# Kernel optimization log

Hardware: AMD Instinct MI355X
Metric: run time of the kernel (lower is better)

The kernel has to match this reference:

```python
import jax, jax.numpy as jnp
import numpy as np

B, T, D = 8, 2048, 1024
NUM_HEADS = 16
SCALE = 1.0 / np.sqrt(D // NUM_HEADS).astype(np.float32)  # sqrt(d_modal//num_heads), per source


def setup_inputs() -> dict:
    key = jax.random.key(0)
    ks = jax.random.split(key, 7)
    s = 1.0 / np.sqrt(D).astype(np.float32)
    return {
        "x": jax.random.normal(ks[0], (B, T, D), dtype=jnp.float32),
        "Wq_w": jax.random.normal(ks[1], (D, D), dtype=jnp.float32) * s,
        "Wq_b": jax.random.normal(ks[2], (D,), dtype=jnp.float32) * 0.01,
        "Wk_w": jax.random.normal(ks[3], (D, D), dtype=jnp.float32) * s,
        "Wk_b": jax.random.normal(ks[4], (D,), dtype=jnp.float32) * 0.01,
        "Wv_w": jax.random.normal(ks[5], (D, D), dtype=jnp.float32) * s,
        "Wv_b": jax.random.normal(ks[6], (D,), dtype=jnp.float32) * 0.01,
    }


def reference(x, Wq_w, Wq_b, Wk_w, Wk_b, Wv_w, Wv_b):
    # Linear projections (torch nn.Linear: y = x @ W.T + b)
    Q = jnp.einsum('btd,ed->bte', x, Wq_w) + Wq_b
    K = jnp.einsum('btd,ed->bte', x, Wk_w) + Wk_b
    V = jnp.einsum('btd,ed->bte', x, Wv_w) + Wv_b
    # scores [B, T, T], scaled by 1/sqrt(d_modal // num_heads) as in source
    scores = jnp.einsum('bqd,bkd->bqk', Q, K) * SCALE
    causal = jnp.tril(jnp.ones((T, T), dtype=bool))  # tril mask buffer
    scores = jnp.where(causal, scores, -jnp.inf)
    attn = jax.nn.softmax(scores, axis=-1)
    return jnp.einsum('bqk,bkd->bqd', attn, V)
```

## Files before the change

kernel.cpp:

```cpp
#include <hip/hip_runtime.h>


typedef float f32x4 __attribute__((ext_vector_type(4)));
typedef _Float16 half8 __attribute__((ext_vector_type(8)));

#define DEVINL __device__ __forceinline__
static constexpr float ATT_SCALE = 0.125f;

DEVINL void gload_lds16(const _Float16* g, _Float16* l) {
  __builtin_amdgcn_global_load_lds((const __attribute__((address_space(1))) void*)g,
                                   (__attribute__((address_space(3))) void*)l, 16, 0, 0);
}

#define SBAR() __builtin_amdgcn_sched_barrier(0)
#define MM(AOFF, BOFF, ASET, BSET) \
  _Pragma("unroll") for (int kk_ = 0; kk_ < 2; ++kk_) \
  _Pragma("unroll") for (int i_ = 0; i_ < 4; ++i_) \
  _Pragma("unroll") for (int jj_ = 0; jj_ < 2; ++jj_) \
    acc[(AOFF) + i_][(BOFF) + jj_] = __builtin_amdgcn_mfma_f32_16x16x32_f16( \
        ASET[i_][kk_], BSET[jj_][kk_], acc[(AOFF) + i_][(BOFF) + jj_], 0, 0, 0);
#define PH_BAR() SBAR(); __builtin_amdgcn_s_barrier(); \
    __builtin_amdgcn_s_setprio(1)
#define PH_DONE() __builtin_amdgcn_s_setprio(0); SBAR()

template <int LDA, int LDB, class GA, class GB>
DEVINL void gemm_core(GA ga, GB gb, int NT, char* ldsb, int tid, f32x4 acc[8][4]) {
  const int l = tid & 63, w = tid >> 6;
  const int wm = w >> 2, wn = w & 3;
  const int lr = l & 15, lk = l >> 4;
  int srow[2], scol[2];
#pragma unroll
  for (int i = 0; i < 2; ++i) {
    const int P = i * 512 + w * 64 + l;
    srow[i] = P >> 3;
    scol[i] = (P & 7) ^ (srow[i] & 7);
  }
  const int ch0 = ((lk ^ (lr & 7)) << 4);
  const int ch1 = (((lk + 4) ^ (lr & 7)) << 4);
  const int abase = lr * 128;
  const int bbase = (wn & 1) * 8192 + lr * 128;

  half8 aA[4][2], aB[4][2], bA[2][2], bB[2][2];

  auto STGA = [&](int t, int h, int bufb) {
    const _Float16* g0 = ga(t, h);
    char* dst = ldsb + bufb * 65536 + h * 16384;
#pragma unroll
    for (int i = 0; i < 2; ++i)
      gload_lds16(g0 + (size_t)srow[i] * LDA + scol[i] * 8,
                  (_Float16*)(dst + i * 8192 + w * 1024));
  };
  auto STGB = [&](int t, int h, int bufb) {
    const _Float16* g0 = gb(t, h);
    char* dst = ldsb + bufb * 65536 + 32768 + h * 16384;
#pragma unroll
    for (int i = 0; i < 2; ++i)
      gload_lds16(g0 + (size_t)srow[i] * LDB + scol[i] * 8,
                  (_Float16*)(dst + i * 8192 + w * 1024));
  };
  auto RDA = [&](int bufb, int ih, half8 d[4][2]) {
    const char* sA = ldsb + bufb * 65536 + wm * 16384 + ih * 8192;
#pragma unroll
    for (int i = 0; i < 4; ++i) {
      d[i][0] = *(const half8*)(sA + abase + i * 2048 + ch0);
      d[i][1] = *(const half8*)(sA + abase + i * 2048 + ch1);
    }
  };
  auto RDB = [&](int bufb, int jh, half8 d[2][2]) {
    const char* sB = ldsb + bufb * 65536 + 32768 + (wn >> 1) * 16384 + jh * 4096;
#pragma unroll
    for (int jj = 0; jj < 2; ++jj) {
      d[jj][0] = *(const half8*)(sB + bbase + jj * 2048 + ch0);
      d[jj][1] = *(const half8*)(sB + bbase + jj * 2048 + ch1);
    }
  };

  auto tile = [&](int t, bool stA, bool stB) {
    const int bufb = t & 1, obuf = bufb ^ 1;
    RDB(bufb, 1, bB);
    if (stA) STGA(t + 1, 0, obuf);
    PH_BAR(); MM(0, 0, aA, bA); PH_DONE();
    RDA(bufb, 1, aB);
    if (stA) STGA(t + 1, 1, obuf);
    PH_BAR(); MM(0, 2, aA, bB); PH_DONE();
    if (stB) STGB(t + 2, 0, bufb);
    SBAR();
    if (stB)      { asm volatile("s_waitcnt vmcnt(2)" ::: "memory"); }
    else if (stA) { asm volatile("s_waitcnt vmcnt(0)" ::: "memory"); }
    PH_BAR(); MM(4, 0, aB, bA); PH_DONE();
    if (stA) { RDA(obuf, 0, aA); RDB(obuf, 0, bA); }
    if (stB) STGB(t + 2, 1, bufb);
    PH_BAR(); MM(4, 2, aB, bB); PH_DONE();
  };

  STGA(0, 0, 0); STGA(0, 1, 0); STGB(0, 0, 0); STGB(0, 1, 0);
  STGB(1, 0, 1); STGB(1, 1, 1);
  asm volatile("s_waitcnt vmcnt(4)" ::: "memory");
  __builtin_amdgcn_s_barrier(); SBAR();
  RDA(0, 0, aA); RDB(0, 0, bA);
  for (int t = 0; t < NT - 2; ++t) tile(t, true, true);
  tile(NT - 2, true, false);
  tile(NT - 1, false, false);
}

__global__ __launch_bounds__(256) void cvt_all(const float* __restrict__ x,
                                               const float* __restrict__ wq,
                                               const float* __restrict__ wk,
                                               const float* __restrict__ wv,
                                               _Float16* __restrict__ xh,
                                               _Float16* __restrict__ wqh,
                                               _Float16* __restrict__ wkh,
                                               _Float16* __restrict__ wvh) {
  const int n8 = 2490368;
  for (int i = blockIdx.x * 256 + threadIdx.x; i < n8; i += 2048 * 256) {
    const float* src; _Float16* dst; int off;
    if (i < 2097152)      { src = x;  dst = xh;  off = i; }
    else if (i < 2228224) { src = wq; dst = wqh; off = i - 2097152; }
    else if (i < 2359296) { src = wk; dst = wkh; off = i - 2228224; }
    else                  { src = wv; dst = wvh; off = i - 2359296; }
    const float4* p = (const float4*)src + (size_t)off * 2;
    float4 v0 = p[0], v1 = p[1];
    half8 h;
    h[0] = (_Float16)v0.x; h[1] = (_Float16)v0.y; h[2] = (_Float16)v0.z; h[3] = (_Float16)v0.w;
    h[4] = (_Float16)v1.x; h[5] = (_Float16)v1.y; h[6] = (_Float16)v1.z; h[7] = (_Float16)v1.w;
    *((half8*)dst + off) = h;
  }
}

__global__ __launch_bounds__(512) void gemm_qkv(
    const _Float16* __restrict__ xh, const _Float16* __restrict__ Wqh,
    const _Float16* __restrict__ Wkh, const _Float16* __restrict__ Wvh,
    const float* __restrict__ bq, const float* __restrict__ bk,
    const float* __restrict__ bv, _Float16* __restrict__ Qh,
    _Float16* __restrict__ Kh, _Float16* __restrict__ VT) {
  __shared__ _Float16 lds[65536];
  const int tid = threadIdx.x;
  const int bid = blockIdx.x;
  const int swz = (bid & 7) * 96 + (bid >> 3);
  const int mt = swz / 12, nt = swz % 12;
  const int sel = nt >> 2;
  const _Float16* Wsel = sel == 0 ? Wqh : (sel == 1 ? Wkh : Wvh);
  const float* bsel = sel == 0 ? bq : (sel == 1 ? bk : bv);
  const _Float16* Ab = xh + (size_t)mt * 256 * 1024;
  const _Float16* Bb = Wsel + (size_t)(nt & 3) * 256 * 1024;
  f32x4 acc[8][4] = {};
  auto ga = [&](int t, int h) { return Ab + (size_t)h * 128 * 1024 + t * 64; };
  auto gb = [&](int t, int h) { return Bb + (size_t)h * 128 * 1024 + t * 64; };
  gemm_core<1024, 1024>(ga, gb, 16, (char*)lds, tid, acc);
  const int l = tid & 63, w = tid >> 6;
  const int wm = w >> 2, wn = w & 3;
  const int lr = l & 15, lk = l >> 4;
  const int n0 = (nt & 3) * 256;
  __syncthreads();
#pragma unroll
  for (int ai = 0; ai < 8; ++ai) {
    const int rbase = wm * 128 + (ai >> 2) * 64 + (ai & 3) * 16 + lk * 4;
#pragma unroll
    for (int j = 0; j < 4; ++j) {
      const int col = wn * 64 + j * 16 + lr;
      const float bvv = bsel[n0 + col];
#pragma unroll
      for (int r = 0; r < 4; ++r) {
        const int row = rbase + r;
        const float v = acc[ai][j][r] + bvv;
        if (sel < 2)
          lds[row * 256 + ((col + (row >> 2) * 16) & 255)] = (_Float16)v;
        else
          lds[col * 256 + ((row + (col >> 2) * 16) & 255)] = (_Float16)v;
      }
    }
  }
  __syncthreads();
#pragma unroll
  for (int i = 0; i < 16; ++i) {
    const int c = i * 512 + tid;
    const int row = c >> 5, c8 = c & 31;
    half8 v = *(const half8*)&lds[row * 256 + ((c8 * 8 + (row >> 2) * 16) & 255)];
    if (sel < 2) {
      _Float16* Out = sel == 0 ? Qh : Kh;
      *(half8*)&Out[(size_t)(mt * 256 + row) * 1024 + n0 + c8 * 8] = v;
    } else {
      const int bb = mt >> 3, t0 = (mt & 7) * 256;
      *(half8*)&VT[((size_t)bb * 1024 + n0 + row) * 2048 + t0 + c8 * 8] = v;
    }
  }
}

__global__ __launch_bounds__(512) void gemm_qk(const _Float16* __restrict__ Qh,
                                               const _Float16* __restrict__ Kh,
                                               float* __restrict__ Sc) {
  __shared__ _Float16 lds[65536];
  const int tid = threadIdx.x;
  const int idx = blockIdx.x, bb = blockIdx.y;
  int qt = 0;
  while ((qt + 1) * (qt + 2) / 2 <= idx) ++qt;
  const int jt = idx - qt * (qt + 1) / 2;
  const _Float16* Ab = Qh + ((size_t)bb * 2048 + qt * 256) * 1024;
  const _Float16* Bb = Kh + ((size_t)bb * 2048 + jt * 256) * 1024;
  f32x4 acc[8][4] = {};
  auto ga = [&](int t, int h) { return Ab + (size_t)h * 128 * 1024 + t * 64; };
  auto gb = [&](int t, int h) { return Bb + (size_t)h * 128 * 1024 + t * 64; };
  gemm_core<1024, 1024>(ga, gb, 16, (char*)lds, tid, acc);
  const int l = tid & 63, w = tid >> 6;
  const int wm = w >> 2, wn = w & 3;
  const int lr = l & 15, lk = l >> 4;
  float* St = Sc + ((size_t)bb * 36 + idx) * 65536;
  const float NINF = -__builtin_inff();
#pragma unroll
  for (int ai = 0; ai < 8; ++ai) {
    const int rbase = wm * 128 + (ai >> 2) * 64 + (ai & 3) * 16 + lk * 4;
#pragma unroll
    for (int j = 0; j < 4; ++j) {
      const int ck = wn * 64 + j * 16 + lr;
      const int kg = jt * 256 + ck;
#pragma unroll
      for (int r = 0; r < 4; ++r) {
        const int rq = rbase + r;
        const int qg = qt * 256 + rq;
        St[(size_t)rq * 256 + ck] = (kg <= qg) ? acc[ai][j][r] * ATT_SCALE : NINF;
      }
    }
  }
}

__global__ __launch_bounds__(256) void softmax_p(const float* __restrict__ Sc,
                                                 _Float16* __restrict__ Pc) {
  const int l = threadIdx.x & 63;
  const int gid = blockIdx.x * 4 + (threadIdx.x >> 6);
  const int b = gid >> 11, q = gid & 2047;
  const int qt = q >> 8, rq = q & 255;
  const int ntile = qt + 1;
  const size_t base = ((size_t)b * 36 + (size_t)(qt * (qt + 1) / 2)) * 65536 +
                      (size_t)rq * 256 + l * 4;
  float vx[32];
  float m = -__builtin_inff();
#pragma unroll
  for (int c = 0; c < 8; ++c) {
    float4 t = {-__builtin_inff(), -__builtin_inff(), -__builtin_inff(), -__builtin_inff()};
    if (c < ntile) t = *(const float4*)&Sc[base + (size_t)c * 65536];
    vx[4 * c] = t.x; vx[4 * c + 1] = t.y; vx[4 * c + 2] = t.z; vx[4 * c + 3] = t.w;
    m = fmaxf(m, fmaxf(fmaxf(t.x, t.y), fmaxf(t.z, t.w)));
  }
#pragma unroll
  for (int s = 1; s < 64; s <<= 1) m = fmaxf(m, __shfl_xor(m, s, 64));
  float sum = 0.f;
#pragma unroll
  for (int i = 0; i < 32; ++i) { vx[i] = __expf(vx[i] - m); sum += vx[i]; }
#pragma unroll
  for (int s = 1; s < 64; s <<= 1) sum += __shfl_xor(sum, s, 64);
  const float inv = 1.f / sum;
  _Float16* Pb = Pc + base;
#pragma unroll
  for (int c = 0; c < 8; ++c) {
    if (c < ntile) {
      _Float16 tmp[4];
      tmp[0] = (_Float16)(vx[4 * c] * inv);
      tmp[1] = (_Float16)(vx[4 * c + 1] * inv);
      tmp[2] = (_Float16)(vx[4 * c + 2] * inv);
      tmp[3] = (_Float16)(vx[4 * c + 3] * inv);
      *(uint64_t*)&Pb[(size_t)c * 65536] = *(const uint64_t*)tmp;
    }
  }
}

__global__ __launch_bounds__(512) void gemm_pv(const _Float16* __restrict__ Pc,
                                               const _Float16* __restrict__ VT,
                                               float* __restrict__ O) {
  __shared__ _Float16 lds[65536];
  const int tid = threadIdx.x;
  const int dt = blockIdx.x, qt = 7 - blockIdx.y, b = blockIdx.z;
  const _Float16* Pb = Pc + ((size_t)b * 36 + (size_t)(qt * (qt + 1) / 2)) * 65536;
  const _Float16* Vb = VT + ((size_t)b * 1024 + dt * 256) * 2048;
  f32x4 acc[8][4] = {};
  auto ga = [&](int t, int h) {
    return Pb + (size_t)(t >> 2) * 65536 + (size_t)h * 128 * 256 + (t & 3) * 64;
  };
  auto gb = [&](int t, int h) { return Vb + (size_t)h * 128 * 2048 + t * 64; };
  gemm_core<256, 2048>(ga, gb, (qt + 1) * 4, (char*)lds, tid, acc);
  const int l = tid & 63, w = tid >> 6;
  const int wm = w >> 2, wn = w & 3;
  const int lr = l & 15, lk = l >> 4;
#pragma unroll
  for (int ai = 0; ai < 8; ++ai) {
    const int rbase = qt * 256 + wm * 128 + (ai >> 2) * 64 + (ai & 3) * 16 + lk * 4;
#pragma unroll
    for (int j = 0; j < 4; ++j) {
      const int cg = dt * 256 + wn * 64 + j * 16 + lr;
#pragma unroll
      for (int r = 0; r < 4; ++r)
        O[((size_t)b * 2048 + rbase + r) * 1024 + cg] = acc[ai][j][r];
    }
  }
}

extern "C" void kernel_launch(void* const* d_in, const int* in_sizes, int n_in,
                              void* d_out, int out_size, void* d_ws, size_t ws_size,
                              hipStream_t stream) {
  const float* x    = (const float*)d_in[0];
  const float* Wq_w = (const float*)d_in[1];
  const float* Wq_b = (const float*)d_in[2];
  const float* Wk_w = (const float*)d_in[3];
  const float* Wk_b = (const float*)d_in[4];
  const float* Wv_w = (const float*)d_in[5];
  const float* Wv_b = (const float*)d_in[6];
  float* out = (float*)d_out;
  char* ws = (char*)d_ws;
  _Float16* xh  = (_Float16*)(ws);
  _Float16* Wqh = (_Float16*)(ws + 33554432);
  _Float16* Wkh = (_Float16*)(ws + 35651584);
  _Float16* Wvh = (_Float16*)(ws + 37748736);
  float*    Sc  = (float*)(ws);
  _Float16* Qh  = (_Float16*)(ws + 75497472);
  _Float16* Kh  = (_Float16*)(ws + 109051904);
  _Float16* Pc  = (_Float16*)(ws + 75497472);
  _Float16* VT  = (_Float16*)(ws + 142606336);

  cvt_all<<<2048, 256, 0, stream>>>(x, Wq_w, Wk_w, Wv_w, xh, Wqh, Wkh, Wvh);
  gemm_qkv<<<768, 512, 0, stream>>>(xh, Wqh, Wkh, Wvh, Wq_b, Wk_b, Wv_b, Qh, Kh, VT);
  gemm_qk<<<dim3(36, 8), 512, 0, stream>>>(Qh, Kh, Sc);
  softmax_p<<<4096, 256, 0, stream>>>(Sc, Pc);
  gemm_pv<<<dim3(4, 8, 8), 512, 0, stream>>>(Pc, VT, out);
}
```

Baseline: 283.8 us.

## Use 256x128 GEMM tiles for QK and PV, store scores as fp16

Adds a new GEMM core with 256x128 output tiles and a simpler double-buffered loop. The QK and PV kernels now use it, which doubles their grid sizes (576 and 512 blocks) for better CU occupancy and load balance on the causal triangle. The score matrix is written and read as fp16 instead of fp32, halving the intermediate traffic through softmax. The trade-offs are lower arithmetic intensity per tile, more barriers per k-step, and reduced precision of the pre-softmax scores.

```diff
diff --git a/kernel.cpp b/kernel.cpp
--- a/kernel.cpp
+++ b/kernel.cpp
@@ -3,6 +3,7 @@
 
 typedef float f32x4 __attribute__((ext_vector_type(4)));
 typedef _Float16 half8 __attribute__((ext_vector_type(8)));
+typedef _Float16 half4 __attribute__((ext_vector_type(4)));
 
 #define DEVINL __device__ __forceinline__
 static constexpr float ATT_SCALE = 0.125f;
@@ -13,6 +14,7 @@
 }
 
 #define SBAR() __builtin_amdgcn_sched_barrier(0)
+
 #define MM(AOFF, BOFF, ASET, BSET) \
   _Pragma("unroll") for (int kk_ = 0; kk_ < 2; ++kk_) \
   _Pragma("unroll") for (int i_ = 0; i_ < 4; ++i_) \
@@ -101,6 +103,88 @@
   for (int t = 0; t < NT - 2; ++t) tile(t, true, true);
   tile(NT - 2, true, false);
   tile(NT - 1, false, false);
+}
+
+template <int LDA, int LDB, class GA, class GB>
+DEVINL void gemm_n128(GA ga, GB gb, int NT, char* ldsb, int tid, f32x4 acc[4][4]) {
+  const int l = tid & 63, w = tid >> 6;
+  const int wm = w >> 1, wn = w & 1;
+  const int lr = l & 15, lk = l >> 4;
+  int srow[2], scol[2];
+#pragma unroll
+  for (int i = 0; i < 2; ++i) {
+    const int P = i * 512 + w * 64 + l;
+    srow[i] = P >> 3;
+    scol[i] = (P & 7) ^ (srow[i] & 7);
+  }
+  const int ch0 = ((lk ^ (lr & 7)) << 4);
+  const int ch1 = (((lk + 4) ^ (lr & 7)) << 4);
+  const int abase = (wm >> 1) * 16384 + ((wm & 1) * 64 + lr) * 128;
+  const int bbase = 32768 + (wn * 64 + lr) * 128;
+
+  auto STG = [&](const _Float16* g0, int ld, int bufb, int slot) {
+    char* dst = ldsb + bufb * 49152 + slot * 16384;
+#pragma unroll
+    for (int i = 0; i < 2; ++i)
+      gload_lds16(g0 + (size_t)srow[i] * ld + scol[i] * 8,
+                  (_Float16*)(dst + i * 8192 + w * 1024));
+  };
+  half8 a[4][2], bfr[4][2];
+  auto RD = [&](int bufb) {
+    const char* bb = ldsb + bufb * 49152;
+#pragma unroll
+    for (int i = 0; i < 4; ++i) {
+      a[i][0] = *(const half8*)(bb + abase + i * 2048 + ch0);
+      a[i][1] = *(const half8*)(bb + abase + i * 2048 + ch1);
+    }
+#pragma unroll
+    for (int j = 0; j < 4; ++j) {
+      bfr[j][0] = *(const half8*)(bb + bbase + j * 2048 + ch0);
+      bfr[j][1] = *(const half8*)(bb + bbase + j * 2048 + ch1);
+    }
+  };
+
+  STG(ga(0, 0), LDA, 0, 0); STG(ga(0, 1), LDA, 0, 1); STG(gb(0), LDB, 0, 2);
+  STG(ga(1, 0), LDA, 1, 0); STG(ga(1, 1), LDA, 1, 1); STG(gb(1), LDB, 1, 2);
+  asm volatile("s_waitcnt vmcnt(6)" ::: "memory");
+  __builtin_amdgcn_s_barrier();
+
+  for (int t = 0; t < NT; ++t) {
+    const int bufb = t & 1;
+    RD(bufb);
+    SBAR();
+    __builtin_amdgcn_s_barrier();
+    asm volatile("s_waitcnt lgkmcnt(0)" ::: "memory");
+    SBAR();
+    __builtin_amdgcn_s_setprio(1);
+#pragma unroll
+    for (int i = 0; i < 4; ++i)
+#pragma unroll
+      for (int j = 0; j < 4; ++j)
+        acc[i][j] = __builtin_amdgcn_mfma_f32_16x16x32_f16(a[i][0], bfr[j][0], acc[i][j], 0, 0, 0);
+    __builtin_amdgcn_s_setprio(0);
+    SBAR();
+    __builtin_amdgcn_s_barrier();
+    if (t + 2 < NT) {
+      STG(ga(t + 2, 0), LDA, bufb, 0);
+      STG(ga(t + 2, 1), LDA, bufb, 1);
+      STG(gb(t + 2), LDB, bufb, 2);
+      asm volatile("s_waitcnt vmcnt(6)" ::: "memory");
+    } else if (t + 1 < NT) {
+      asm volatile("s_waitcnt vmcnt(0)" ::: "memory");
+    }
+    SBAR();
+    __builtin_amdgcn_s_barrier();
+    __builtin_amdgcn_s_setprio(1);
+#pragma unroll
+    for (int i = 0; i < 4; ++i)
+#pragma unroll
+      for (int j = 0; j < 4; ++j)
+        acc[i][j] = __builtin_amdgcn_mfma_f32_16x16x32_f16(a[i][1], bfr[j][1], acc[i][j], 0, 0, 0);
+    __builtin_amdgcn_s_setprio(0);
+    SBAR();
+    __builtin_amdgcn_s_barrier();
+  }
 }
 
 __global__ __launch_bounds__(256) void cvt_all(const float* __restrict__ x,
@@ -188,42 +272,44 @@
 
 __global__ __launch_bounds__(512) void gemm_qk(const _Float16* __restrict__ Qh,
                                                const _Float16* __restrict__ Kh,
-                                               float* __restrict__ Sc) {
-  __shared__ _Float16 lds[65536];
+                                               _Float16* __restrict__ Sc) {
+  __shared__ _Float16 lds[49152];
   const int tid = threadIdx.x;
-  const int idx = blockIdx.x, bb = blockIdx.y;
-  int qt = 0;
-  while ((qt + 1) * (qt + 2) / 2 <= idx) ++qt;
-  const int jt = idx - qt * (qt + 1) / 2;
-  const _Float16* Ab = Qh + ((size_t)bb * 2048 + qt * 256) * 1024;
-  const _Float16* Bb = Kh + ((size_t)bb * 2048 + jt * 256) * 1024;
-  f32x4 acc[8][4] = {};
+  const int j = blockIdx.x;
+  const int b = j / 72, r = j % 72;
+  int qt = 0, cum = 0;
+  while (cum + (qt + 1) * 2 <= r) { cum += (qt + 1) * 2; ++qt; }
+  const int jn = r - cum;
+  const _Float16* Ab = Qh + ((size_t)b * 2048 + qt * 256) * 1024;
+  const _Float16* Bb = Kh + ((size_t)b * 2048 + jn * 128) * 1024;
+  f32x4 acc[4][4] = {};
   auto ga = [&](int t, int h) { return Ab + (size_t)h * 128 * 1024 + t * 64; };
-  auto gb = [&](int t, int h) { return Bb + (size_t)h * 128 * 1024 + t * 64; };
-  gemm_core<1024, 1024>(ga, gb, 16, (char*)lds, tid, acc);
+  auto gb = [&](int t) { return Bb + t * 64; };
+  gemm_n128<1024, 1024>(ga, gb, 16, (char*)lds, tid, acc);
   const int l = tid & 63, w = tid >> 6;
-  const int wm = w >> 2, wn = w & 3;
+  const int wm = w >> 1, wn = w & 1;
   const int lr = l & 15, lk = l >> 4;
-  float* St = Sc + ((size_t)bb * 36 + idx) * 65536;
-  const float NINF = -__builtin_inff();
-#pragma unroll
-  for (int ai = 0; ai < 8; ++ai) {
-    const int rbase = wm * 128 + (ai >> 2) * 64 + (ai & 3) * 16 + lk * 4;
-#pragma unroll
-    for (int j = 0; j < 4; ++j) {
-      const int ck = wn * 64 + j * 16 + lr;
-      const int kg = jt * 256 + ck;
-#pragma unroll
-      for (int r = 0; r < 4; ++r) {
-        const int rq = rbase + r;
-        const int qg = qt * 256 + rq;
-        St[(size_t)rq * 256 + ck] = (kg <= qg) ? acc[ai][j][r] * ATT_SCALE : NINF;
+  _Float16* St = Sc + ((size_t)b * 36 + (size_t)(qt * (qt + 1) / 2) + (jn >> 1)) * 65536 +
+                 (jn & 1) * 128;
+  const _Float16 NINF = (_Float16)(-__builtin_inff());
+#pragma unroll
+  for (int i = 0; i < 4; ++i) {
+#pragma unroll
+    for (int jj = 0; jj < 4; ++jj) {
+      const int col = wn * 64 + jj * 16 + lr;
+      const int kg = jn * 128 + col;
+#pragma unroll
+      for (int rr = 0; rr < 4; ++rr) {
+        const int row = wm * 64 + i * 16 + lk * 4 + rr;
+        const int qg = qt * 256 + row;
+        St[(size_t)row * 256 + col] =
+            (kg <= qg) ? (_Float16)(acc[i][jj][rr] * ATT_SCALE) : NINF;
       }
     }
   }
 }
 
-__global__ __launch_bounds__(256) void softmax_p(const float* __restrict__ Sc,
+__global__ __launch_bounds__(256) void softmax_p(const _Float16* __restrict__ Sc,
                                                  _Float16* __restrict__ Pc) {
   const int l = threadIdx.x & 63;
   const int gid = blockIdx.x * 4 + (threadIdx.x >> 6);
@@ -236,10 +322,13 @@
   float m = -__builtin_inff();
 #pragma unroll
   for (int c = 0; c < 8; ++c) {
-    float4 t = {-__builtin_inff(), -__builtin_inff(), -__builtin_inff(), -__builtin_inff()};
-    if (c < ntile) t = *(const float4*)&Sc[base + (size_t)c * 65536];
-    vx[4 * c] = t.x; vx[4 * c + 1] = t.y; vx[4 * c + 2] = t.z; vx[4 * c + 3] = t.w;
-    m = fmaxf(m, fmaxf(fmaxf(t.x, t.y), fmaxf(t.z, t.w)));
+    float x0 = -__builtin_inff(), x1 = x0, x2 = x0, x3 = x0;
+    if (c < ntile) {
+      half4 t = *(const half4*)&Sc[base + (size_t)c * 65536];
+      x0 = (float)t[0]; x1 = (float)t[1]; x2 = (float)t[2]; x3 = (float)t[3];
+    }
+    vx[4 * c] = x0; vx[4 * c + 1] = x1; vx[4 * c + 2] = x2; vx[4 * c + 3] = x3;
+    m = fmaxf(m, fmaxf(fmaxf(x0, x1), fmaxf(x2, x3)));
   }
 #pragma unroll
   for (int s = 1; s < 64; s <<= 1) m = fmaxf(m, __shfl_xor(m, s, 64));
@@ -253,12 +342,12 @@
 #pragma unroll
   for (int c = 0; c < 8; ++c) {
     if (c < ntile) {
-      _Float16 tmp[4];
-      tmp[0] = (_Float16)(vx[4 * c] * inv);
-      tmp[1] = (_Float16)(vx[4 * c + 1] * inv);
-      tmp[2] = (_Float16)(vx[4 * c + 2] * inv);
-      tmp[3] = (_Float16)(vx[4 * c + 3] * inv);
-      *(uint64_t*)&Pb[(size_t)c * 65536] = *(const uint64_t*)tmp;
+      half4 p;
+      p[0] = (_Float16)(vx[4 * c] * inv);
+      p[1] = (_Float16)(vx[4 * c + 1] * inv);
+      p[2] = (_Float16)(vx[4 * c + 2] * inv);
+      p[3] = (_Float16)(vx[4 * c + 3] * inv);
+      *(half4*)&Pb[(size_t)c * 65536] = p;
     }
   }
 }
@@ -266,29 +355,32 @@
 __global__ __launch_bounds__(512) void gemm_pv(const _Float16* __restrict__ Pc,
                                                const _Float16* __restrict__ VT,
                                                float* __restrict__ O) {
-  __shared__ _Float16 lds[65536];
+  __shared__ _Float16 lds[49152];
   const int tid = threadIdx.x;
-  const int dt = blockIdx.x, qt = 7 - blockIdx.y, b = blockIdx.z;
+  const int j = blockIdx.x;
+  const int qt = 7 - (j >> 6);
+  const int dt = (j >> 3) & 7, b = j & 7;
   const _Float16* Pb = Pc + ((size_t)b * 36 + (size_t)(qt * (qt + 1) / 2)) * 65536;
-  const _Float16* Vb = VT + ((size_t)b * 1024 + dt * 256) * 2048;
-  f32x4 acc[8][4] = {};
+  const _Float16* Vb = VT + ((size_t)b * 1024 + dt * 128) * 2048;
+  f32x4 acc[4][4] = {};
   auto ga = [&](int t, int h) {
-    return Pb + (size_t)(t >> 2) * 65536 + (size_t)h * 128 * 256 + (t & 3) * 64;
-  };
-  auto gb = [&](int t, int h) { return Vb + (size_t)h * 128 * 2048 + t * 64; };
-  gemm_core<256, 2048>(ga, gb, (qt + 1) * 4, (char*)lds, tid, acc);
+    return Pb + (size_t)(t >> 2) * 65536 + (size_t)h * 32768 + (t & 3) * 64;
+  };
+  auto gb = [&](int t) { return Vb + t * 64; };
+  gemm_n128<256, 2048>(ga, gb, (qt + 1) * 4, (char*)lds, tid, acc);
   const int l = tid & 63, w = tid >> 6;
-  const int wm = w >> 2, wn = w & 3;
+  const int wm = w >> 1, wn = w & 1;
   const int lr = l & 15, lk = l >> 4;
 #pragma unroll
-  for (int ai = 0; ai < 8; ++ai) {
-    const int rbase = qt * 256 + wm * 128 + (ai >> 2) * 64 + (ai & 3) * 16 + lk * 4;
-#pragma unroll
-    for (int j = 0; j < 4; ++j) {
-      const int cg = dt * 256 + wn * 64 + j * 16 + lr;
-#pragma unroll
-      for (int r = 0; r < 4; ++r)
-        O[((size_t)b * 2048 + rbase + r) * 1024 + cg] = acc[ai][j][r];
+  for (int i = 0; i < 4; ++i) {
+#pragma unroll
+    for (int jj = 0; jj < 4; ++jj) {
+      const int cg = dt * 128 + wn * 64 + jj * 16 + lr;
+#pragma unroll
+      for (int rr = 0; rr < 4; ++rr) {
+        const int rg = qt * 256 + wm * 64 + i * 16 + lk * 4 + rr;
+        O[((size_t)b * 2048 + rg) * 1024 + cg] = acc[i][jj][rr];
+      }
     }
   }
 }
@@ -309,7 +401,7 @@
   _Float16* Wqh = (_Float16*)(ws + 33554432);
   _Float16* Wkh = (_Float16*)(ws + 35651584);
   _Float16* Wvh = (_Float16*)(ws + 37748736);
-  float*    Sc  = (float*)(ws);
+  _Float16* Sc  = (_Float16*)(ws);
   _Float16* Qh  = (_Float16*)(ws + 75497472);
   _Float16* Kh  = (_Float16*)(ws + 109051904);
   _Float16* Pc  = (_Float16*)(ws + 75497472);
@@ -317,7 +409,7 @@
 
   cvt_all<<<2048, 256, 0, stream>>>(x, Wq_w, Wk_w, Wv_w, xh, Wqh, Wkh, Wvh);
   gemm_qkv<<<768, 512, 0, stream>>>(xh, Wqh, Wkh, Wvh, Wq_b, Wk_b, Wv_b, Qh, Kh, VT);
-  gemm_qk<<<dim3(36, 8), 512, 0, stream>>>(Qh, Kh, Sc);
+  gemm_qk<<<576, 512, 0, stream>>>(Qh, Kh, Sc);
   softmax_p<<<4096, 256, 0, stream>>>(Sc, Pc);
-  gemm_pv<<<dim3(4, 8, 8), 512, 0, stream>>>(Pc, VT, out);
-}
+  gemm_pv<<<512, 512, 0, stream>>>(Pc, VT, out);
+}
```

Result: faster. 275.4 us (-3.0%).
